# Performance work log

Hardware: AMD Instinct MI355X
Metric: run time of the kernel (lower is better)

## Reference

```python
import jax, jax.numpy as jnp
import numpy as np

DIM, HEADS, SEQ_LEN = 768, 12, 4096
HEAD_DIM = DIM // HEADS
RMS_EPS = 1.1920928955078125e-07  # torch fp32 finfo eps (default for F.rms_norm)
ATTN_SCALE = 0.12


def _rms_norm(x):
    # F.rms_norm(x, (x.size(-1),)) with no weight
    return x * jax.lax.rsqrt(jnp.mean(x * x, axis=-1, keepdims=True) + RMS_EPS)


def _rotary_tables(T, head_dim):
    # angular_freq: (1/1024)**linspace(0,1,head_dim//4) padded with zeros to head_dim//2
    freqs = (1.0 / 1024.0) ** jnp.linspace(0.0, 1.0, head_dim // 4, dtype=jnp.float32)
    freqs = jnp.concatenate([freqs, jnp.zeros(head_dim // 4, dtype=jnp.float32)])
    t = jnp.arange(T, dtype=jnp.float32)
    theta = t[:, None] * freqs[None, :]  # [T, head_dim//2]
    return jnp.cos(theta), jnp.sin(theta)


def _apply_rotary(x, cos, sin):
    # x: [B, T, H, D]; cos/sin: [T, D//2]
    x1, x2 = jnp.split(x.astype(jnp.float32), 2, axis=-1)
    c = cos[None, :, None, :]
    s = sin[None, :, None, :]
    y1 = x1 * c + x2 * s
    y2 = -x1 * s + x2 * c
    return jnp.concatenate([y1, y2], axis=-1).astype(x.dtype)


def setup_inputs() -> dict:
    key = jax.random.key(0)
    k1, k2, k3 = jax.random.split(key, 3)
    x = jax.random.normal(k1, (1, SEQ_LEN, DIM), dtype=jnp.float32)
    std = 0.5 * DIM ** (-0.5)
    bound = (3.0 ** 0.5) * std
    qkv_w = jax.random.uniform(k2, (3, DIM, DIM), dtype=jnp.float32, minval=-bound, maxval=bound)
    # c_proj is zero-initialized in the module; use small random weights for a nontrivial baseline
    c_proj_w = jax.random.normal(k3, (DIM, DIM), dtype=jnp.float32) * (DIM ** -0.5)
    return {"x": x, "qkv_w": qkv_w, "c_proj_w": c_proj_w}


def reference(x, qkv_w, c_proj_w):
    B, T, dim = x.shape
    H, D = HEADS, HEAD_DIM
    # fused QKV: F.linear(x, qkv_w.flatten(end_dim=1)) -> x @ W^T, split into q,k,v
    qkv = jnp.einsum('btd,kfd->btkf', x, qkv_w)  # [B, T, 3, dim]
    qkv = qkv.reshape(B, T, 3, H, D)
    q, k, v = qkv[:, :, 0], qkv[:, :, 1], qkv[:, :, 2]  # each [B, T, H, D]
    q, k = _rms_norm(q), _rms_norm(k)
    cos, sin = _rotary_tables(T, D)
    q, k = _apply_rotary(q, cos, sin), _apply_rotary(k, cos, sin)
    # causal attention with scale=0.12 (flex_attention with causal block mask)
    scores = jnp.einsum('bthd,bshd->bhts', q, k) * ATTN_SCALE  # [B, H, T, T]
    causal = jnp.tril(jnp.ones((T, T), dtype=bool))
    scores = jnp.where(causal[None, None], scores, jnp.finfo(scores.dtype).min)
    probs = jax.nn.softmax(scores, axis=-1)
    y = jnp.einsum('bhts,bshd->bthd', probs, v).reshape(B, T, dim)
    return y @ c_proj_w.T
```

## Files before the change

### kernel.cpp

```cpp
#include <hip/hip_runtime.h>
#include <math.h>


typedef __bf16 bf16;
typedef __bf16 bf16x4 __attribute__((ext_vector_type(4)));
typedef __bf16 bf16x8 __attribute__((ext_vector_type(8)));
typedef float  f32x4  __attribute__((ext_vector_type(4)));

#define MFMA_BF16(a, b, c) __builtin_amdgcn_mfma_f32_16x16x32_bf16((a), (b), (c), 0, 0, 0)

#define SEQ  4096
#define NH   12
#define HD   64
#define DM   768
#define NQKV 2304
#define NPART 4
#define ATTN_SCALE 0.12f
#define LOG2E 1.4426950408889634f
#define RMS_EPS 1.1920928955078125e-07f

typedef __attribute__((address_space(3))) void  lds_void;
typedef const __attribute__((address_space(1))) void g_void;

__device__ __forceinline__ void gload16(const void* g, void* l)
{
  __builtin_amdgcn_global_load_lds((g_void*)g, (lds_void*)l, 16, 0, 0);
}

__global__ __launch_bounds__(256) void convert_all(
    const float* __restrict__ s0, bf16* __restrict__ d0, int n0,
    const float* __restrict__ s1, bf16* __restrict__ d1, int n1,
    const float* __restrict__ s2, bf16* __restrict__ d2, int n2)
{
  int b = blockIdx.x;
  const int b0 = n0 >> 11, b1 = n1 >> 11;
  const float* s; bf16* d;
  if (b < b0)            { s = s0; d = d0; }
  else if (b < b0 + b1)  { s = s1; d = d1; b -= b0; }
  else                   { s = s2; d = d2; b -= b0 + b1; }
  const int i0 = (b * 256 + threadIdx.x) * 8;
  f32x4 a = *(const f32x4*)(s + i0);
  f32x4 c = *(const f32x4*)(s + i0 + 4);
  bf16x8 o;
#pragma unroll
  for (int j = 0; j < 4; j++) { o[j] = (bf16)a[j]; o[j + 4] = (bf16)c[j]; }
  *(bf16x8*)(d + i0) = o;
}

__device__ __forceinline__ void gemm128_core(
    const bf16* __restrict__ A, const bf16* __restrict__ B,
    int m0, int n0, bf16 (*As)[128][32], bf16 (*Bs)[128][32], f32x4 acc[4][4])
{
  const int tid = threadIdx.x;
  const int lane = tid & 63, w = tid >> 6;
  const int c16 = lane & 15, q4 = lane >> 4;
  const int mo = (w & 1) * 64, no = (w >> 1) * 64;
  const int srow = tid >> 2, scol = (tid & 3) * 8;
  const f32x4 vzero = {0.f, 0.f, 0.f, 0.f};
#pragma unroll
  for (int i = 0; i < 4; i++)
#pragma unroll
    for (int j = 0; j < 4; j++) acc[i][j] = vzero;

  const bf16* aBase = A + (size_t)(m0 + srow) * DM + scol;
  const bf16* bBase = B + (size_t)(n0 + srow) * DM + scol;

#define STAGE128(buf, kk) do {                                          \
    gload16(aBase + (kk),                   &As[buf][srow][scol]);      \
    gload16(aBase + (size_t)64 * DM + (kk), &As[buf][srow + 64][scol]); \
    gload16(bBase + (kk),                   &Bs[buf][srow][scol]);      \
    gload16(bBase + (size_t)64 * DM + (kk), &Bs[buf][srow + 64][scol]); \
  } while (0)

  STAGE128(0, 0);
  __syncthreads();
  int cur = 0;
  for (int k0 = 0; k0 < DM; k0 += 32) {
    const int kn = k0 + 32;
    if (kn < DM) STAGE128(cur ^ 1, kn);
    bf16x8 ar[4], br[4];
#pragma unroll
    for (int mq = 0; mq < 4; mq++)
      ar[mq] = *(const bf16x8*)&As[cur][mo + mq * 16 + c16][q4 * 8];
#pragma unroll
    for (int nq = 0; nq < 4; nq++)
      br[nq] = *(const bf16x8*)&Bs[cur][no + nq * 16 + c16][q4 * 8];
    __builtin_amdgcn_s_setprio(1);
#pragma unroll
    for (int mq = 0; mq < 4; mq++)
#pragma unroll
      for (int nq = 0; nq < 4; nq++)
        acc[mq][nq] = MFMA_BF16(ar[mq], br[nq], acc[mq][nq]);
    __builtin_amdgcn_s_setprio(0);
    __syncthreads();
    cur ^= 1;
  }
#undef STAGE128
}

__global__ __launch_bounds__(256) void gemm_qkv(
    const bf16* __restrict__ A, const bf16* __restrict__ B,
    bf16* __restrict__ Qb, bf16* __restrict__ Kb, bf16* __restrict__ Vt)
{
  __shared__ bf16 As[2][128][32];
  __shared__ bf16 Bs[2][128][32];
  const int m0 = blockIdx.x * 128, n0 = blockIdx.y * 128;
  f32x4 acc[4][4];
  gemm128_core(A, B, m0, n0, As, Bs, acc);

  const int lane = threadIdx.x & 63, w = threadIdx.x >> 6;
  const int c16 = lane & 15, q4 = lane >> 4;
  const int mo = (w & 1) * 64, no = (w >> 1) * 64;
  const int kidx = blockIdx.y / 6;
  const int rr0 = (n0 - kidx * DM) + no;
  const int h = rr0 >> 6;

  if (kidx == 2) {
#pragma unroll
    for (int nq = 0; nq < 4; nq++) {
      const int d = nq * 16 + c16;
#pragma unroll
      for (int mq = 0; mq < 4; mq++) {
        const int mb = m0 + mo + mq * 16 + q4 * 4;
#pragma unroll
        for (int rg = 0; rg < 4; rg++)
          Vt[((h * HD) + d) * SEQ + mb + rg] = (bf16)acc[mq][nq][rg];
      }
    }
  } else {
    bf16* dst = kidx ? Kb : Qb;
    const float scale = kidx ? 1.0f : (ATTN_SCALE * LOG2E);
    const float fr = exp2f(-10.0f * (float)c16 * (1.0f / 15.0f));
#pragma unroll
    for (int mq = 0; mq < 4; mq++) {
#pragma unroll
      for (int rg = 0; rg < 4; rg++) {
        const int m = m0 + mo + mq * 16 + q4 * 4 + rg;
        const float x0 = acc[mq][0][rg], x1 = acc[mq][1][rg];
        const float x2 = acc[mq][2][rg], x3 = acc[mq][3][rg];
        float ss = x0 * x0 + x1 * x1 + x2 * x2 + x3 * x3;
        ss += __shfl_xor(ss, 1, 64);
        ss += __shfl_xor(ss, 2, 64);
        ss += __shfl_xor(ss, 4, 64);
        ss += __shfl_xor(ss, 8, 64);
        const float rinv = rsqrtf(ss * (1.0f / 64.0f) + RMS_EPS) * scale;
        const float xn0 = x0 * rinv, xn1 = x1 * rinv;
        const float xn2 = x2 * rinv, xn3 = x3 * rinv;
        float sn, cs;
        sincosf((float)m * fr, &sn, &cs);
        const float y0 = xn0 * cs + xn2 * sn;
        const float y2 = xn2 * cs - xn0 * sn;
        bf16* rp = dst + (size_t)(h * SEQ + m) * HD + c16;
        rp[0]  = (bf16)y0;
        rp[16] = (bf16)xn1;
        rp[32] = (bf16)y2;
        rp[48] = (bf16)xn3;
      }
    }
  }
}

__global__ __launch_bounds__(256) void gemm_proj(
    const bf16* __restrict__ A, const bf16* __restrict__ B, float* __restrict__ C)
{
  __shared__ bf16 As[2][64][32];
  __shared__ bf16 Bs[2][64][32];
  const int m0 = blockIdx.x * 64, n0 = blockIdx.y * 64;
  const int tid = threadIdx.x;
  const int lane = tid & 63, w = tid >> 6;
  const int c16 = lane & 15, q4 = lane >> 4;
  const int mo = (w & 1) * 32, no = (w >> 1) * 32;
  const int srow = tid >> 2, scol = (tid & 3) * 8;
  const f32x4 vzero = {0.f, 0.f, 0.f, 0.f};
  f32x4 acc[2][2];
#pragma unroll
  for (int i = 0; i < 2; i++)
#pragma unroll
    for (int j = 0; j < 2; j++) acc[i][j] = vzero;

  const bf16* aBase = A + (size_t)(m0 + srow) * DM + scol;
  const bf16* bBase = B + (size_t)(n0 + srow) * DM + scol;

#define STAGE64(buf, kk) do {                          \
    gload16(aBase + (kk), &As[buf][srow][scol]);       \
    gload16(bBase + (kk), &Bs[buf][srow][scol]);       \
  } while (0)

  STAGE64(0, 0);
  __syncthreads();
  int cur = 0;
  for (int k0 = 0; k0 < DM; k0 += 32) {
    const int kn = k0 + 32;
    if (kn < DM) STAGE64(cur ^ 1, kn);
    bf16x8 ar[2], br[2];
#pragma unroll
    for (int mq = 0; mq < 2; mq++)
      ar[mq] = *(const bf16x8*)&As[cur][mo + mq * 16 + c16][q4 * 8];
#pragma unroll
    for (int nq = 0; nq < 2; nq++)
      br[nq] = *(const bf16x8*)&Bs[cur][no + nq * 16 + c16][q4 * 8];
    __builtin_amdgcn_s_setprio(1);
#pragma unroll
    for (int mq = 0; mq < 2; mq++)
#pragma unroll
      for (int nq = 0; nq < 2; nq++)
        acc[mq][nq] = MFMA_BF16(ar[mq], br[nq], acc[mq][nq]);
    __builtin_amdgcn_s_setprio(0);
    __syncthreads();
    cur ^= 1;
  }
#undef STAGE64

#pragma unroll
  for (int nq = 0; nq < 2; nq++) {
    const int n = n0 + no + nq * 16 + c16;
#pragma unroll
    for (int mq = 0; mq < 2; mq++) {
      const int mb = m0 + mo + mq * 16 + q4 * 4;
#pragma unroll
      for (int rg = 0; rg < 4; rg++)
        C[(size_t)(mb + rg) * DM + n] = acc[mq][nq][rg];
    }
  }
}

__global__ __launch_bounds__(256, 3) void flash_partial(
    const bf16* __restrict__ Qb, const bf16* __restrict__ Kb,
    const bf16* __restrict__ Vt, bf16* __restrict__ Opart,
    float* __restrict__ Lpart)
{
  __shared__ bf16 Ks[64][72];
  __shared__ bf16 Vts[64][72];
  __shared__ bf16 Pst[4][32][68];
  const int id = blockIdx.x;
  const int swz = (id & 7) * 96 + (id >> 3);
  const int h = swz >> 6;
  const int rrem = swz & 63;
  const int p = rrem >> 4;
  const int jb = rrem & 15;
  const int tid = threadIdx.x;
  const int lane = tid & 63, w = tid >> 6;
  const int c16 = lane & 15, q4 = lane >> 4;
  const int sr = tid >> 3, sc8 = (tid & 7) * 8;

  const bf16* Kbase = Kb + (size_t)h * SEQ * HD;
  const bf16* Vbase = Vt + (size_t)h * HD * SEQ;
  const f32x4 vzero = {0.f, 0.f, 0.f, 0.f};

#pragma unroll 1
  for (int half = 0; half < 2; ++half) {
    const int qi = half ? jb : (31 - jb);
    const int q0 = qi * 128;

    bf16x8 aq[2][2];
#pragma unroll
    for (int f = 0; f < 2; f++) {
      const int tq = q0 + w * 32 + f * 16 + c16;
      aq[f][0] = *(const bf16x8*)&Qb[((h * SEQ) + tq) * HD + q4 * 8];
      aq[f][1] = *(const bf16x8*)&Qb[((h * SEQ) + tq) * HD + 32 + q4 * 8];
    }
    const int qg[2] = { q0 + w * 32 + c16, q0 + w * 32 + 16 + c16 };
    const int qb[2] = { q0 + w * 32,       q0 + w * 32 + 16 };

    f32x4 O[2][4];
    float l_f[2] = {0.f, 0.f};
#pragma unroll
    for (int f = 0; f < 2; f++)
#pragma unroll
      for (int j = 0; j < 4; j++) O[f][j] = vzero;

    const int sEnd = q0 + 64;
    const int sBeg = p * 64;
    if (sBeg <= sEnd) {
      bf16x8 kr0 = *(const bf16x8*)&Kbase[(sBeg + sr) * HD + sc8];
      bf16x8 kr1 = *(const bf16x8*)&Kbase[(sBeg + sr + 32) * HD + sc8];
      bf16x8 vr0 = *(const bf16x8*)&Vbase[sr * SEQ + sBeg + sc8];
      bf16x8 vr1 = *(const bf16x8*)&Vbase[(sr + 32) * SEQ + sBeg + sc8];

      for (int s0 = sBeg; s0 <= sEnd; s0 += NPART * 64) {
        __syncthreads();
        *(bf16x8*)&Ks[sr][sc8]       = kr0;
        *(bf16x8*)&Ks[sr + 32][sc8]  = kr1;
        *(bf16x8*)&Vts[sr][sc8]      = vr0;
        *(bf16x8*)&Vts[sr + 32][sc8] = vr1;
        __syncthreads();

        const int snext = s0 + NPART * 64;
        if (snext <= sEnd) {
          kr0 = *(const bf16x8*)&Kbase[(snext + sr) * HD + sc8];
          kr1 = *(const bf16x8*)&Kbase[(snext + sr + 32) * HD + sc8];
          vr0 = *(const bf16x8*)&Vbase[sr * SEQ + snext + sc8];
          vr1 = *(const bf16x8*)&Vbase[(sr + 32) * SEQ + snext + sc8];
        }

        bf16x8 kf0[4], kf1[4];
#pragma unroll
        for (int nt = 0; nt < 4; nt++) {
          kf0[nt] = *(const bf16x8*)&Ks[nt * 16 + c16][q4 * 8];
          kf1[nt] = *(const bf16x8*)&Ks[nt * 16 + c16][32 + q4 * 8];
        }
#pragma unroll
        for (int f = 0; f < 2; f++) {
          f32x4 S[4];
          __builtin_amdgcn_s_setprio(1);
#pragma unroll
          for (int nt = 0; nt < 4; nt++) {
            f32x4 z = vzero;
            z = MFMA_BF16(kf0[nt], aq[f][0], z);
            z = MFMA_BF16(kf1[nt], aq[f][1], z);
            S[nt] = z;
          }
          __builtin_amdgcn_s_setprio(0);
          float lf = l_f[f];
          if (s0 + 63 <= qb[f]) {
#pragma unroll
            for (int nt = 0; nt < 4; nt++) {
#pragma unroll
              for (int rg = 0; rg < 4; rg++) {
                const float pv = exp2f(S[nt][rg]);
                S[nt][rg] = pv;
                lf += pv;
              }
              bf16x4 pk = { (bf16)S[nt][0], (bf16)S[nt][1], (bf16)S[nt][2], (bf16)S[nt][3] };
              *(bf16x4*)&Pst[w][f * 16 + c16][nt * 16 + q4 * 4] = pk;
            }
          } else if (s0 > qb[f] + 15) {
            const bf16x4 zk = { (bf16)0.f, (bf16)0.f, (bf16)0.f, (bf16)0.f };
#pragma unroll
            for (int nt = 0; nt < 4; nt++)
              *(bf16x4*)&Pst[w][f * 16 + c16][nt * 16 + q4 * 4] = zk;
          } else {
#pragma unroll
            for (int nt = 0; nt < 4; nt++) {
#pragma unroll
              for (int rg = 0; rg < 4; rg++) {
                const int s_g = s0 + nt * 16 + q4 * 4 + rg;
                const float pv = (s_g > qg[f]) ? 0.f : exp2f(S[nt][rg]);
                S[nt][rg] = pv;
                lf += pv;
              }
              bf16x4 pk = { (bf16)S[nt][0], (bf16)S[nt][1], (bf16)S[nt][2], (bf16)S[nt][3] };
              *(bf16x4*)&Pst[w][f * 16 + c16][nt * 16 + q4 * 4] = pk;
            }
          }
          l_f[f] = lf;
        }
        bf16x8 ap[2][2];
#pragma unroll
        for (int f = 0; f < 2; f++) {
          ap[f][0] = *(const bf16x8*)&Pst[w][f * 16 + c16][q4 * 8];
          ap[f][1] = *(const bf16x8*)&Pst[w][f * 16 + c16][32 + q4 * 8];
        }
#pragma unroll
        for (int dt = 0; dt < 4; dt++) {
          bf16x8 bv0 = *(const bf16x8*)&Vts[dt * 16 + c16][q4 * 8];
          bf16x8 bv1 = *(const bf16x8*)&Vts[dt * 16 + c16][32 + q4 * 8];
          __builtin_amdgcn_s_setprio(1);
#pragma unroll
          for (int f = 0; f < 2; f++) {
            O[f][dt] = MFMA_BF16(ap[f][0], bv0, O[f][dt]);
            O[f][dt] = MFMA_BF16(ap[f][1], bv1, O[f][dt]);
          }
          __builtin_amdgcn_s_setprio(0);
        }
      }
    }

#pragma unroll
    for (int f = 0; f < 2; f++) {
      float l = l_f[f];
      l += __shfl_xor(l, 16, 64);
      l += __shfl_xor(l, 32, 64);
      l_f[f] = l;
    }
    const int u = ((h * 32 + qi) * NPART + p);
    bf16* Op = Opart + (size_t)u * 8192;
#pragma unroll
    for (int f = 0; f < 2; f++)
#pragma unroll
      for (int dt = 0; dt < 4; dt++)
#pragma unroll
        for (int rg = 0; rg < 4; rg++)
          Op[(w * 32 + f * 16 + q4 * 4 + rg) * 64 + dt * 16 + c16] = (bf16)O[f][dt][rg];
    if (lane < 32) {
      if (q4 == 0) {
#pragma unroll
        for (int f = 0; f < 2; f++)
          Lpart[u * 128 + w * 32 + f * 16 + c16] = l_f[f];
      }
    }
  }
}

__global__ __launch_bounds__(256) void flash_combine(
    const bf16* __restrict__ Opart, const float* __restrict__ Lpart,
    bf16* __restrict__ Y)
{
  const int q64 = blockIdx.x, h = blockIdx.y;
  const int qi = q64 >> 1, roff = (q64 & 1) * 64;
  const int row = threadIdx.x >> 2, cg = (threadIdx.x & 3) * 16;
  const int u0 = (h * 32 + qi) * NPART;
  const int r128 = roff + row;
  float lsum = 0.f;
#pragma unroll
  for (int p = 0; p < NPART; p++) lsum += Lpart[(u0 + p) * 128 + r128];
  const float inv = 1.0f / lsum;
  const bf16* O0 = Opart + (size_t)u0 * 8192 + r128 * 64 + cg;
  bf16* yp = Y + (size_t)(q64 * 64 + row) * DM + h * HD + cg;
#pragma unroll
  for (int j = 0; j < 16; j += 8) {
    float s[8] = {0, 0, 0, 0, 0, 0, 0, 0};
#pragma unroll
    for (int p = 0; p < NPART; p++) {
      bf16x8 a = *(const bf16x8*)(O0 + p * 8192 + j);
#pragma unroll
      for (int e = 0; e < 8; e++) s[e] += (float)a[e];
    }
#pragma unroll
    for (int e = 0; e < 8; e++) yp[j + e] = (bf16)(s[e] * inv);
  }
}

extern "C" void kernel_launch(void* const* d_in, const int* in_sizes, int n_in,
                              void* d_out, int out_size, void* d_ws, size_t ws_size,
                              hipStream_t stream)
{
  (void)in_sizes; (void)n_in; (void)out_size; (void)ws_size;
  const float* x      = (const float*)d_in[0];
  const float* qkvw   = (const float*)d_in[1];
  const float* cprojw = (const float*)d_in[2];
  float* outp = (float*)d_out;

  const int NX = SEQ * DM, NW = NQKV * DM, NP = DM * DM;

  char* ws = (char*)d_ws;
  bf16*  xb    = (bf16*)(ws);
  bf16*  wqkv  = (bf16*)(ws + 6291456);
  bf16*  wproj = (bf16*)(ws + 9830400);
  bf16*  Q     = (bf16*)(ws + 11010048);
  bf16*  K     = (bf16*)(ws + 17301504);
  bf16*  Vt    = (bf16*)(ws + 23592960);
  bf16*  Y     = (bf16*)(ws + 29884416);
  bf16*  Opart = (bf16*)(ws + 36175872);
  float* Lpart = (float*)(ws + 61341696);

  convert_all<<<dim3((NX + NW + NP) / 2048), 256, 0, stream>>>(
      x, xb, NX, qkvw, wqkv, NW, cprojw, wproj, NP);

  gemm_qkv     <<<dim3(SEQ / 128, NQKV / 128), 256, 0, stream>>>(xb, wqkv, Q, K, Vt);
  flash_partial<<<dim3(16 * NH * NPART),       256, 0, stream>>>(Q, K, Vt, Opart, Lpart);
  flash_combine<<<dim3(SEQ / 64, NH),          256, 0, stream>>>(Opart, Lpart, Y);
  gemm_proj    <<<dim3(SEQ / 64, DM / 64),     256, 0, stream>>>(Y, wproj, outp);
}
```

Measured before the change: 161.9 us.

## Triple-buffer GEMM LDS staging with explicit vmcnt waits for deeper prefetch

The QKV and output-projection GEMMs move from double-buffered to triple-buffered LDS staging, keeping two K-tiles of global-to-LDS loads in flight. Each step waits with an explicit vmcnt count and a raw s_barrier instead of __syncthreads, which drains every outstanding load. The goal is to hide more global-load latency behind the MFMA work. In exchange, LDS use per block grows by half, and correctness now depends on the hand-computed vmcnt counts matching the number of loads each stage issues.

```diff
diff --git a/kernel.cpp b/kernel.cpp
--- a/kernel.cpp
+++ b/kernel.cpp
@@ -65,26 +65,33 @@
   const bf16* aBase = A + (size_t)(m0 + srow) * DM + scol;
   const bf16* bBase = B + (size_t)(n0 + srow) * DM + scol;
 
-#define STAGE128(buf, kk) do {                                          \
+#define STG128(buf, kk) do {                                            \
     gload16(aBase + (kk),                   &As[buf][srow][scol]);      \
     gload16(aBase + (size_t)64 * DM + (kk), &As[buf][srow + 64][scol]); \
     gload16(bBase + (kk),                   &Bs[buf][srow][scol]);      \
     gload16(bBase + (size_t)64 * DM + (kk), &Bs[buf][srow + 64][scol]); \
   } while (0)
 
-  STAGE128(0, 0);
-  __syncthreads();
-  int cur = 0;
-  for (int k0 = 0; k0 < DM; k0 += 32) {
-    const int kn = k0 + 32;
-    if (kn < DM) STAGE128(cur ^ 1, kn);
+  const int NT = DM / 32;
+  STG128(0, 0);
+  STG128(1, 32);
+#pragma unroll 3
+  for (int u = 0; u < NT; ++u) {
+    if (u + 2 < NT) STG128((u + 2) % 3, (u + 2) * 32);
+    const int nfly = (NT - 1 - u) < 2 ? (NT - 1 - u) : 2;
+    if (nfly == 2)      asm volatile("s_waitcnt vmcnt(8)" ::: "memory");
+    else if (nfly == 1) asm volatile("s_waitcnt vmcnt(4)" ::: "memory");
+    else                asm volatile("s_waitcnt vmcnt(0)" ::: "memory");
+    __builtin_amdgcn_sched_barrier(0);
+    __builtin_amdgcn_s_barrier();
+    const int cb = u % 3;
     bf16x8 ar[4], br[4];
 #pragma unroll
     for (int mq = 0; mq < 4; mq++)
-      ar[mq] = *(const bf16x8*)&As[cur][mo + mq * 16 + c16][q4 * 8];
+      ar[mq] = *(const bf16x8*)&As[cb][mo + mq * 16 + c16][q4 * 8];
 #pragma unroll
     for (int nq = 0; nq < 4; nq++)
-      br[nq] = *(const bf16x8*)&Bs[cur][no + nq * 16 + c16][q4 * 8];
+      br[nq] = *(const bf16x8*)&Bs[cb][no + nq * 16 + c16][q4 * 8];
     __builtin_amdgcn_s_setprio(1);
 #pragma unroll
     for (int mq = 0; mq < 4; mq++)
@@ -92,18 +99,19 @@
       for (int nq = 0; nq < 4; nq++)
         acc[mq][nq] = MFMA_BF16(ar[mq], br[nq], acc[mq][nq]);
     __builtin_amdgcn_s_setprio(0);
-    __syncthreads();
-    cur ^= 1;
-  }
-#undef STAGE128
+    asm volatile("s_waitcnt lgkmcnt(0)" ::: "memory");
+    __builtin_amdgcn_sched_barrier(0);
+    __builtin_amdgcn_s_barrier();
+  }
+#undef STG128
 }
 
 __global__ __launch_bounds__(256) void gemm_qkv(
     const bf16* __restrict__ A, const bf16* __restrict__ B,
     bf16* __restrict__ Qb, bf16* __restrict__ Kb, bf16* __restrict__ Vt)
 {
-  __shared__ bf16 As[2][128][32];
-  __shared__ bf16 Bs[2][128][32];
+  __shared__ bf16 As[3][128][32];
+  __shared__ bf16 Bs[3][128][32];
   const int m0 = blockIdx.x * 128, n0 = blockIdx.y * 128;
   f32x4 acc[4][4];
   gemm128_core(A, B, m0, n0, As, Bs, acc);
@@ -163,8 +171,8 @@
 __global__ __launch_bounds__(256) void gemm_proj(
     const bf16* __restrict__ A, const bf16* __restrict__ B, float* __restrict__ C)
 {
-  __shared__ bf16 As[2][64][32];
-  __shared__ bf16 Bs[2][64][32];
+  __shared__ bf16 As[3][64][32];
+  __shared__ bf16 Bs[3][64][32];
   const int m0 = blockIdx.x * 64, n0 = blockIdx.y * 64;
   const int tid = threadIdx.x;
   const int lane = tid & 63, w = tid >> 6;
@@ -181,24 +189,31 @@
   const bf16* aBase = A + (size_t)(m0 + srow) * DM + scol;
   const bf16* bBase = B + (size_t)(n0 + srow) * DM + scol;
 
-#define STAGE64(buf, kk) do {                          \
+#define STG64(buf, kk) do {                            \
     gload16(aBase + (kk), &As[buf][srow][scol]);       \
     gload16(bBase + (kk), &Bs[buf][srow][scol]);       \
   } while (0)
 
-  STAGE64(0, 0);
-  __syncthreads();
-  int cur = 0;
-  for (int k0 = 0; k0 < DM; k0 += 32) {
-    const int kn = k0 + 32;
-    if (kn < DM) STAGE64(cur ^ 1, kn);
+  const int NT = DM / 32;
+  STG64(0, 0);
+  STG64(1, 32);
+#pragma unroll 3
+  for (int u = 0; u < NT; ++u) {
+    if (u + 2 < NT) STG64((u + 2) % 3, (u + 2) * 32);
+    const int nfly = (NT - 1 - u) < 2 ? (NT - 1 - u) : 2;
+    if (nfly == 2)      asm volatile("s_waitcnt vmcnt(4)" ::: "memory");
+    else if (nfly == 1) asm volatile("s_waitcnt vmcnt(2)" ::: "memory");
+    else                asm volatile("s_waitcnt vmcnt(0)" ::: "memory");
+    __builtin_amdgcn_sched_barrier(0);
+    __builtin_amdgcn_s_barrier();
+    const int cb = u % 3;
     bf16x8 ar[2], br[2];
 #pragma unroll
     for (int mq = 0; mq < 2; mq++)
-      ar[mq] = *(const bf16x8*)&As[cur][mo + mq * 16 + c16][q4 * 8];
+      ar[mq] = *(const bf16x8*)&As[cb][mo + mq * 16 + c16][q4 * 8];
 #pragma unroll
     for (int nq = 0; nq < 2; nq++)
-      br[nq] = *(const bf16x8*)&Bs[cur][no + nq * 16 + c16][q4 * 8];
+      br[nq] = *(const bf16x8*)&Bs[cb][no + nq * 16 + c16][q4 * 8];
     __builtin_amdgcn_s_setprio(1);
 #pragma unroll
     for (int mq = 0; mq < 2; mq++)
@@ -206,10 +221,11 @@
       for (int nq = 0; nq < 2; nq++)
         acc[mq][nq] = MFMA_BF16(ar[mq], br[nq], acc[mq][nq]);
     __builtin_amdgcn_s_setprio(0);
-    __syncthreads();
-    cur ^= 1;
-  }
-#undef STAGE64
+    asm volatile("s_waitcnt lgkmcnt(0)" ::: "memory");
+    __builtin_amdgcn_sched_barrier(0);
+    __builtin_amdgcn_s_barrier();
+  }
+#undef STG64
 
 #pragma unroll
   for (int nq = 0; nq < 2; nq++) {
```

After: 171.8 us. +6.1%, slower.

## Fuse flash-attention partial combine into output projection GEMM A-tile loading

Applied to the files above, without the earlier changes.

Removes the separate flash_combine kernel and instead has gemm_proj read the four partial O tiles directly, sum them, scale by the inverse row sum (precomputed into shared memory from Lpart), and write the combined bf16 tile into LDS. This drops one kernel launch and the round trip of writing and rereading the Y buffer. In exchange, each of the 12 column-tile blocks redundantly re-reads and re-reduces the 4x partial data, and the A loads become register-staged rather than async direct-to-LDS, adding latency inside the k-loop.

```diff
diff --git a/kernel.cpp b/kernel.cpp
--- a/kernel.cpp
+++ b/kernel.cpp
@@ -161,16 +161,21 @@
 }
 
 __global__ __launch_bounds__(256) void gemm_proj(
-    const bf16* __restrict__ A, const bf16* __restrict__ B, float* __restrict__ C)
+    const bf16* __restrict__ Opart, const float* __restrict__ Lpart,
+    const bf16* __restrict__ B, float* __restrict__ C)
 {
   __shared__ bf16 As[2][64][32];
   __shared__ bf16 Bs[2][64][32];
+  __shared__ float invs[NH * 64];
   const int m0 = blockIdx.x * 64, n0 = blockIdx.y * 64;
   const int tid = threadIdx.x;
   const int lane = tid & 63, w = tid >> 6;
   const int c16 = lane & 15, q4 = lane >> 4;
   const int mo = (w & 1) * 32, no = (w >> 1) * 32;
   const int srow = tid >> 2, scol = (tid & 3) * 8;
+  const int qi = m0 >> 7;
+  const int rbase = m0 & 64;
+  const int r128 = rbase + srow;
   const f32x4 vzero = {0.f, 0.f, 0.f, 0.f};
   f32x4 acc[2][2];
 #pragma unroll
@@ -178,20 +183,50 @@
 #pragma unroll
     for (int j = 0; j < 2; j++) acc[i][j] = vzero;
 
-  const bf16* aBase = A + (size_t)(m0 + srow) * DM + scol;
   const bf16* bBase = B + (size_t)(n0 + srow) * DM + scol;
 
-#define STAGE64(buf, kk) do {                          \
-    gload16(aBase + (kk), &As[buf][srow][scol]);       \
-    gload16(bBase + (kk), &Bs[buf][srow][scol]);       \
+#define ALOAD(kk, r0, r1, r2, r3) do {                                        \
+    const int h_ = (kk) >> 6;                                                 \
+    const bf16* ab_ = Opart + (size_t)((h_ * 32 + qi) * NPART) * 8192         \
+                      + r128 * 64 + ((kk) & 63) + scol;                       \
+    r0 = *(const bf16x8*)(ab_);                                               \
+    r1 = *(const bf16x8*)(ab_ + 8192);                                        \
+    r2 = *(const bf16x8*)(ab_ + 16384);                                       \
+    r3 = *(const bf16x8*)(ab_ + 24576);                                       \
   } while (0)
 
-  STAGE64(0, 0);
+#define AWRITE(buf, kk, r0, r1, r2, r3) do {                                  \
+    const float iv_ = invs[(((kk) >> 6) << 6) + srow];                        \
+    bf16x8 y_;                                                                \
+    _Pragma("unroll")                                                         \
+    for (int e = 0; e < 8; e++)                                               \
+      y_[e] = (bf16)(((float)r0[e] + (float)r1[e] + (float)r2[e]              \
+                      + (float)r3[e]) * iv_);                                 \
+    *(bf16x8*)&As[buf][srow][scol] = y_;                                      \
+  } while (0)
+
+  bf16x8 p0, p1, p2, p3;
+  ALOAD(0, p0, p1, p2, p3);
+  gload16(bBase, &Bs[0][srow][scol]);
+  for (int idx = tid; idx < NH * 64; idx += 256) {
+    const int h = idx >> 6, r = idx & 63;
+    const int u0 = (h * 32 + qi) * NPART;
+    float ls = 0.f;
+#pragma unroll
+    for (int p = 0; p < NPART; p++) ls += Lpart[(u0 + p) * 128 + rbase + r];
+    invs[idx] = 1.0f / ls;
+  }
   __syncthreads();
+  AWRITE(0, 0, p0, p1, p2, p3);
+  __syncthreads();
+
   int cur = 0;
   for (int k0 = 0; k0 < DM; k0 += 32) {
     const int kn = k0 + 32;
-    if (kn < DM) STAGE64(cur ^ 1, kn);
+    if (kn < DM) {
+      ALOAD(kn, p0, p1, p2, p3);
+      gload16(bBase + kn, &Bs[cur ^ 1][srow][scol]);
+    }
     bf16x8 ar[2], br[2];
 #pragma unroll
     for (int mq = 0; mq < 2; mq++)
@@ -206,10 +241,12 @@
       for (int nq = 0; nq < 2; nq++)
         acc[mq][nq] = MFMA_BF16(ar[mq], br[nq], acc[mq][nq]);
     __builtin_amdgcn_s_setprio(0);
+    if (kn < DM) AWRITE(cur ^ 1, kn, p0, p1, p2, p3);
     __syncthreads();
     cur ^= 1;
   }
-#undef STAGE64
+#undef ALOAD
+#undef AWRITE
 
 #pragma unroll
   for (int nq = 0; nq < 2; nq++) {
@@ -392,35 +429,6 @@
   }
 }
 
-__global__ __launch_bounds__(256) void flash_combine(
-    const bf16* __restrict__ Opart, const float* __restrict__ Lpart,
-    bf16* __restrict__ Y)
-{
-  const int q64 = blockIdx.x, h = blockIdx.y;
-  const int qi = q64 >> 1, roff = (q64 & 1) * 64;
-  const int row = threadIdx.x >> 2, cg = (threadIdx.x & 3) * 16;
-  const int u0 = (h * 32 + qi) * NPART;
-  const int r128 = roff + row;
-  float lsum = 0.f;
-#pragma unroll
-  for (int p = 0; p < NPART; p++) lsum += Lpart[(u0 + p) * 128 + r128];
-  const float inv = 1.0f / lsum;
-  const bf16* O0 = Opart + (size_t)u0 * 8192 + r128 * 64 + cg;
-  bf16* yp = Y + (size_t)(q64 * 64 + row) * DM + h * HD + cg;
-#pragma unroll
-  for (int j = 0; j < 16; j += 8) {
-    float s[8] = {0, 0, 0, 0, 0, 0, 0, 0};
-#pragma unroll
-    for (int p = 0; p < NPART; p++) {
-      bf16x8 a = *(const bf16x8*)(O0 + p * 8192 + j);
-#pragma unroll
-      for (int e = 0; e < 8; e++) s[e] += (float)a[e];
-    }
-#pragma unroll
-    for (int e = 0; e < 8; e++) yp[j + e] = (bf16)(s[e] * inv);
-  }
-}
-
 extern "C" void kernel_launch(void* const* d_in, const int* in_sizes, int n_in,
                               void* d_out, int out_size, void* d_ws, size_t ws_size,
                               hipStream_t stream)
@@ -440,15 +448,13 @@
   bf16*  Q     = (bf16*)(ws + 11010048);
   bf16*  K     = (bf16*)(ws + 17301504);
   bf16*  Vt    = (bf16*)(ws + 23592960);
-  bf16*  Y     = (bf16*)(ws + 29884416);
-  bf16*  Opart = (bf16*)(ws + 36175872);
-  float* Lpart = (float*)(ws + 61341696);
+  bf16*  Opart = (bf16*)(ws + 29884416);
+  float* Lpart = (float*)(ws + 55050240);
 
   convert_all<<<dim3((NX + NW + NP) / 2048), 256, 0, stream>>>(
       x, xb, NX, qkvw, wqkv, NW, cprojw, wproj, NP);
 
   gemm_qkv     <<<dim3(SEQ / 128, NQKV / 128), 256, 0, stream>>>(xb, wqkv, Q, K, Vt);
   flash_partial<<<dim3(16 * NH * NPART),       256, 0, stream>>>(Q, K, Vt, Opart, Lpart);
-  flash_combine<<<dim3(SEQ / 64, NH),          256, 0, stream>>>(Opart, Lpart, Y);
-  gemm_proj    <<<dim3(SEQ / 64, DM / 64),     256, 0, stream>>>(Y, wproj, outp);
-}
+  gemm_proj    <<<dim3(SEQ / 64, DM / 64),     256, 0, stream>>>(Opart, Lpart, wproj, outp);
+}
```

Result: slower. 168.4 us (+4.0%).

## Double-buffer K/V tiles with direct-to-LDS loads, XOR swizzle, MFMA row sums

Applied to the files above, without the earlier changes.

Replaces the register-staged K/V tile loads with direct global-to-LDS loads (gload16) into a double-buffered, XOR-swizzled LDS layout. The next tile is fetched during compute, and one barrier per iteration is removed. The softmax denominator is now computed by an extra MFMA against a ones column instead of scalar adds and cross-lane shuffles. In exchange, LDS use grows from two padded tiles to four unpadded ones, which may affect occupancy, and the row sums come from bf16-rounded probabilities.

```diff
diff --git a/kernel.cpp b/kernel.cpp
--- a/kernel.cpp
+++ b/kernel.cpp
@@ -229,8 +229,8 @@
     const bf16* __restrict__ Vt, bf16* __restrict__ Opart,
     float* __restrict__ Lpart)
 {
-  __shared__ bf16 Ks[64][72];
-  __shared__ bf16 Vts[64][72];
+  __shared__ bf16 Ks[2][64][64];
+  __shared__ bf16 Vts[2][64][64];
   __shared__ bf16 Pst[4][32][68];
   const int id = blockIdx.x;
   const int swz = (id & 7) * 96 + (id >> 3);
@@ -241,11 +241,26 @@
   const int tid = threadIdx.x;
   const int lane = tid & 63, w = tid >> 6;
   const int c16 = lane & 15, q4 = lane >> 4;
-  const int sr = tid >> 3, sc8 = (tid & 7) * 8;
+  const int sr = tid >> 3;
+  const int scS = (((tid & 7) ^ (sr & 7))) * 8;
+  const int sdst = (tid & 7) * 8;
+  const int rsw = c16 & 7;
 
   const bf16* Kbase = Kb + (size_t)h * SEQ * HD;
   const bf16* Vbase = Vt + (size_t)h * HD * SEQ;
   const f32x4 vzero = {0.f, 0.f, 0.f, 0.f};
+
+#define FSTAGE(buf, ss) do {                                                   \
+    gload16(&Kbase[(size_t)((ss) + sr) * HD + scS],       &Ks[buf][sr][sdst]); \
+    gload16(&Kbase[(size_t)((ss) + sr + 32) * HD + scS],  &Ks[buf][sr + 32][sdst]); \
+    gload16(&Vbase[(size_t)sr * SEQ + (ss) + scS],        &Vts[buf][sr][sdst]); \
+    gload16(&Vbase[(size_t)(sr + 32) * SEQ + (ss) + scS], &Vts[buf][sr + 32][sdst]); \
+  } while (0)
+
+  const bf16 bv1c = (c16 == 0) ? (bf16)1.0f : (bf16)0.0f;
+  bf16x8 bone;
+#pragma unroll
+  for (int e = 0; e < 8; e++) bone[e] = bv1c;
 
 #pragma unroll 1
   for (int half = 0; half < 2; ++half) {
@@ -263,7 +278,7 @@
     const int qb[2] = { q0 + w * 32,       q0 + w * 32 + 16 };
 
     f32x4 O[2][4];
-    float l_f[2] = {0.f, 0.f};
+    f32x4 acc_l[2] = {vzero, vzero};
 #pragma unroll
     for (int f = 0; f < 2; f++)
 #pragma unroll
@@ -272,32 +287,19 @@
     const int sEnd = q0 + 64;
     const int sBeg = p * 64;
     if (sBeg <= sEnd) {
-      bf16x8 kr0 = *(const bf16x8*)&Kbase[(sBeg + sr) * HD + sc8];
-      bf16x8 kr1 = *(const bf16x8*)&Kbase[(sBeg + sr + 32) * HD + sc8];
-      bf16x8 vr0 = *(const bf16x8*)&Vbase[sr * SEQ + sBeg + sc8];
-      bf16x8 vr1 = *(const bf16x8*)&Vbase[(sr + 32) * SEQ + sBeg + sc8];
+      FSTAGE(0, sBeg);
+      __syncthreads();
+      int cur = 0;
 
       for (int s0 = sBeg; s0 <= sEnd; s0 += NPART * 64) {
-        __syncthreads();
-        *(bf16x8*)&Ks[sr][sc8]       = kr0;
-        *(bf16x8*)&Ks[sr + 32][sc8]  = kr1;
-        *(bf16x8*)&Vts[sr][sc8]      = vr0;
-        *(bf16x8*)&Vts[sr + 32][sc8] = vr1;
-        __syncthreads();
-
         const int snext = s0 + NPART * 64;
-        if (snext <= sEnd) {
-          kr0 = *(const bf16x8*)&Kbase[(snext + sr) * HD + sc8];
-          kr1 = *(const bf16x8*)&Kbase[(snext + sr + 32) * HD + sc8];
-          vr0 = *(const bf16x8*)&Vbase[sr * SEQ + snext + sc8];
-          vr1 = *(const bf16x8*)&Vbase[(sr + 32) * SEQ + snext + sc8];
-        }
+        if (snext <= sEnd) FSTAGE(cur ^ 1, snext);
 
         bf16x8 kf0[4], kf1[4];
 #pragma unroll
         for (int nt = 0; nt < 4; nt++) {
-          kf0[nt] = *(const bf16x8*)&Ks[nt * 16 + c16][q4 * 8];
-          kf1[nt] = *(const bf16x8*)&Ks[nt * 16 + c16][32 + q4 * 8];
+          kf0[nt] = *(const bf16x8*)&Ks[cur][nt * 16 + c16][(q4 ^ rsw) * 8];
+          kf1[nt] = *(const bf16x8*)&Ks[cur][nt * 16 + c16][((q4 + 4) ^ rsw) * 8];
         }
 #pragma unroll
         for (int f = 0; f < 2; f++) {
@@ -311,16 +313,11 @@
             S[nt] = z;
           }
           __builtin_amdgcn_s_setprio(0);
-          float lf = l_f[f];
           if (s0 + 63 <= qb[f]) {
 #pragma unroll
             for (int nt = 0; nt < 4; nt++) {
 #pragma unroll
-              for (int rg = 0; rg < 4; rg++) {
-                const float pv = exp2f(S[nt][rg]);
-                S[nt][rg] = pv;
-                lf += pv;
-              }
+              for (int rg = 0; rg < 4; rg++) S[nt][rg] = exp2f(S[nt][rg]);
               bf16x4 pk = { (bf16)S[nt][0], (bf16)S[nt][1], (bf16)S[nt][2], (bf16)S[nt][3] };
               *(bf16x4*)&Pst[w][f * 16 + c16][nt * 16 + q4 * 4] = pk;
             }
@@ -335,15 +332,12 @@
 #pragma unroll
               for (int rg = 0; rg < 4; rg++) {
                 const int s_g = s0 + nt * 16 + q4 * 4 + rg;
-                const float pv = (s_g > qg[f]) ? 0.f : exp2f(S[nt][rg]);
-                S[nt][rg] = pv;
-                lf += pv;
+                S[nt][rg] = (s_g > qg[f]) ? 0.f : exp2f(S[nt][rg]);
               }
               bf16x4 pk = { (bf16)S[nt][0], (bf16)S[nt][1], (bf16)S[nt][2], (bf16)S[nt][3] };
               *(bf16x4*)&Pst[w][f * 16 + c16][nt * 16 + q4 * 4] = pk;
             }
           }
-          l_f[f] = lf;
         }
         bf16x8 ap[2][2];
 #pragma unroll
@@ -352,27 +346,27 @@
           ap[f][1] = *(const bf16x8*)&Pst[w][f * 16 + c16][32 + q4 * 8];
         }
 #pragma unroll
+        for (int f = 0; f < 2; f++) {
+          acc_l[f] = MFMA_BF16(ap[f][0], bone, acc_l[f]);
+          acc_l[f] = MFMA_BF16(ap[f][1], bone, acc_l[f]);
+        }
+#pragma unroll
         for (int dt = 0; dt < 4; dt++) {
-          bf16x8 bv0 = *(const bf16x8*)&Vts[dt * 16 + c16][q4 * 8];
-          bf16x8 bv1 = *(const bf16x8*)&Vts[dt * 16 + c16][32 + q4 * 8];
+          bf16x8 bv0 = *(const bf16x8*)&Vts[cur][dt * 16 + c16][(q4 ^ rsw) * 8];
+          bf16x8 bw1 = *(const bf16x8*)&Vts[cur][dt * 16 + c16][((q4 + 4) ^ rsw) * 8];
           __builtin_amdgcn_s_setprio(1);
 #pragma unroll
           for (int f = 0; f < 2; f++) {
             O[f][dt] = MFMA_BF16(ap[f][0], bv0, O[f][dt]);
-            O[f][dt] = MFMA_BF16(ap[f][1], bv1, O[f][dt]);
+            O[f][dt] = MFMA_BF16(ap[f][1], bw1, O[f][dt]);
           }
           __builtin_amdgcn_s_setprio(0);
         }
+        __syncthreads();
+        cur ^= 1;
       }
     }
 
-#pragma unroll
-    for (int f = 0; f < 2; f++) {
-      float l = l_f[f];
-      l += __shfl_xor(l, 16, 64);
-      l += __shfl_xor(l, 32, 64);
-      l_f[f] = l;
-    }
     const int u = ((h * 32 + qi) * NPART + p);
     bf16* Op = Opart + (size_t)u * 8192;
 #pragma unroll
@@ -382,14 +376,15 @@
 #pragma unroll
         for (int rg = 0; rg < 4; rg++)
           Op[(w * 32 + f * 16 + q4 * 4 + rg) * 64 + dt * 16 + c16] = (bf16)O[f][dt][rg];
-    if (lane < 32) {
-      if (q4 == 0) {
-#pragma unroll
-        for (int f = 0; f < 2; f++)
-          Lpart[u * 128 + w * 32 + f * 16 + c16] = l_f[f];
-      }
-    }
-  }
+    if (c16 == 0) {
+#pragma unroll
+      for (int f = 0; f < 2; f++)
+#pragma unroll
+        for (int rg = 0; rg < 4; rg++)
+          Lpart[u * 128 + w * 32 + f * 16 + q4 * 4 + rg] = acc_l[f][rg];
+    }
+  }
+#undef FSTAGE
 }
 
 __global__ __launch_bounds__(256) void flash_combine(
```

Result: no change. 160.8 us (-0.7%).
